# Performance work log

Hardware: AMD Instinct MI355X
Metric: run time of the kernel (lower is better)

Reference implementation:

```python
import jax, jax.numpy as jnp
import numpy as np
from jax.scipy.linalg import expm

LAMBDA_ORTHO = 1.0


def setup_inputs() -> dict:
    key = jax.random.key(0)
    so8_raw = jax.random.normal(key, (524288, 8, 8), dtype=jnp.float32)
    return {"so8_raw": so8_raw}


def reference(so8_raw):
    # A = 0.5 * (P - P^T): skew-symmetric part per 8x8 block
    A = 0.5 * (so8_raw - jnp.swapaxes(so8_raw, -1, -2))
    # R = expm(A), batched over leading dim via vmap
    R = jax.vmap(expm)(A)
    # ||R^T R - I||_F per block, then mean over blocks
    gram = jnp.einsum('nji,njk->nik', R, R)  # R^T R, [N,8,8]
    err = gram - jnp.eye(8, dtype=R.dtype)
    ortho_err = jnp.sqrt(jnp.sum(err * err, axis=(1, 2))).mean()
    return LAMBDA_ORTHO * ortho_err
```

## Files before the change

### kernel.cpp

```cpp
#include <hip/hip_runtime.h>
#include <math.h>

#pragma clang fp contract(off)

typedef float f2 __attribute__((ext_vector_type(2)));

static __device__ __forceinline__ f2 sp(float x) { f2 r; r.x = x; r.y = x; return r; }
#define FMA2(A, B, C) __builtin_elementwise_fma((A), (B), (C))

#define EL(m, i, j) (m[(i)*4 + ((j) >> 1)][(j) & 1])

__device__ __forceinline__ void mm8p(const f2* __restrict__ A,
                                     const f2* __restrict__ B,
                                     f2* __restrict__ C) {
  #pragma unroll
  for (int i = 0; i < 8; ++i) {
    #pragma unroll
    for (int c = 0; c < 4; ++c) {
      f2 s = sp(EL(A, i, 0)) * B[0*4 + c];
      #pragma unroll
      for (int k = 1; k < 8; ++k)
        s = FMA2(sp(EL(A, i, k)), B[k*4 + c], s);
      C[i*4 + c] = s;
    }
  }
}

__global__ __launch_bounds__(256, 1)
void triality_kernel(const float* __restrict__ in, double* __restrict__ acc)
{
  const int t = blockIdx.x * 256 + threadIdx.x;
  const float4* src = (const float4*)(in + (size_t)t * 64);

  float p[64];
  #pragma unroll
  for (int i = 0; i < 16; ++i) {
    float4 q4 = src[i];
    p[4*i+0] = q4.x; p[4*i+1] = q4.y; p[4*i+2] = q4.z; p[4*i+3] = q4.w;
  }

  f2 aa[32];
  #pragma unroll
  for (int i = 0; i < 8; ++i)
    #pragma unroll
    for (int j = 0; j < 8; ++j)
      EL(aa, i, j) = 0.5f * (p[i*8+j] - p[j*8+i]);

  float l1 = 0.0f;
  #pragma unroll
  for (int j = 0; j < 8; ++j) {
    float cs = 0.0f;
    #pragma unroll
    for (int i = 0; i < 8; ++i) cs = cs + fabsf(EL(aa, i, j));
    l1 = fmaxf(l1, cs);
  }

  float fl = floorf(log2f(l1 / 3.925724783138660f));
  int ns = (fl > 0.0f) ? (int)fl : 0;
  if (ns > 0) {
    f2 sc = sp(exp2f((float)(-ns)));
    #pragma unroll
    for (int e = 0; e < 32; ++e) aa[e] = aa[e] * sc;
  }

  f2 a2[32];
  #pragma unroll
  for (int i = 0; i < 8; ++i)
    #pragma unroll
    for (int c = 0; c < 4; ++c) {
      f2 s = sp(EL(aa, i, 0)) * aa[0*4 + c];
      #pragma unroll
      for (int k = 1; k < 8; ++k)
        s = FMA2(sp(EL(aa, i, k)), aa[k*4 + c], s);
      a2[i*4 + c] = s;
    }

  f2 a4[32];
  #pragma unroll
  for (int i = 0; i < 8; ++i)
    #pragma unroll
    for (int c = 0; c < 4; ++c) {
      f2 s = sp(EL(a2, i, 0)) * a2[0*4 + c];
      #pragma unroll
      for (int k = 1; k < 8; ++k)
        s = FMA2(sp(EL(a2, i, k)), a2[k*4 + c], s);
      a4[i*4 + c] = s;
    }

  f2 w6[32];
  #pragma unroll
  for (int i = 0; i < 8; ++i)
    #pragma unroll
    for (int c = 0; c < 4; ++c) {
      f2 s = sp(EL(a4, i, 0)) * a2[0*4 + c];
      #pragma unroll
      for (int k = 1; k < 8; ++k)
        s = FMA2(sp(EL(a4, i, k)), a2[k*4 + c], s);
      w6[i*4 + c] = s;
    }

  f2 vv[32];
  #pragma unroll
  for (int e = 0; e < 32; ++e) {
    f2 x6 = w6[e], x4 = a4[e], x2 = a2[e];
    f2 w = FMA2(sp(1512.0f), x4, x6);
    w = FMA2(sp(277200.0f), x2, w);
    f2 v = FMA2(sp(56.0f), x6, sp(25200.0f) * x4);
    v = FMA2(sp(1995840.0f), x2, v);
    w6[e] = w; vv[e] = v;
  }
  #pragma unroll
  for (int i = 0; i < 8; ++i) {
    EL(w6, i, i) = EL(w6, i, i) + 8648640.0f;
    EL(vv, i, i) = EL(vv, i, i) + 17297280.0f;
  }

  f2 uu[32];
  #pragma unroll
  for (int i = 0; i < 8; ++i)
    #pragma unroll
    for (int c = 0; c < 4; ++c) {
      f2 s = sp(EL(aa, i, 0)) * w6[0*4 + c];
      #pragma unroll
      for (int k = 1; k < 8; ++k)
        s = FMA2(sp(EL(aa, i, k)), w6[k*4 + c], s);
      uu[i*4 + c] = s;
    }

  #pragma unroll
  for (int e = 0; e < 32; ++e) {
    f2 U = uu[e], V = vv[e];
    uu[e] = U + V;
    vv[e] = V - U;
  }
  f2* P = uu;
  f2* Q = vv;

  #pragma unroll
  for (int k = 0; k < 8; ++k) {
    float amax = fabsf(EL(Q, k, k)); int jp = k;
    #pragma unroll
    for (int i = k+1; i < 8; ++i) {
      float av = fabsf(EL(Q, i, k));
      if (av > amax) { amax = av; jp = i; }
    }
    #pragma unroll
    for (int i = k+1; i < 8; ++i) {
      bool d = (jp == i);
      #pragma unroll
      for (int j = 0; j < 8; ++j) {
        float x = EL(Q, k, j), y = EL(Q, i, j);
        EL(Q, k, j) = d ? y : x;
        EL(Q, i, j) = d ? x : y;
        float px = EL(P, k, j), py = EL(P, i, j);
        EL(P, k, j) = d ? py : px;
        EL(P, i, j) = d ? px : py;
      }
    }
    float dk = EL(Q, k, k);
    #pragma unroll
    for (int i = k+1; i < 8; ++i) EL(Q, i, k) = EL(Q, i, k) / dk;
    #pragma unroll
    for (int i = k+1; i < 8; ++i) {
      float lik = EL(Q, i, k);
      #pragma unroll
      for (int j = k+1; j < 8; ++j)
        EL(Q, i, j) = __builtin_fmaf(-lik, EL(Q, k, j), EL(Q, i, j));
      f2 nl = sp(-lik);
      #pragma unroll
      for (int c = 0; c < 4; ++c)
        P[i*4 + c] = FMA2(nl, P[k*4 + c], P[i*4 + c]);
    }
  }

  #pragma unroll
  for (int k = 7; k >= 0; --k) {
    float dk = EL(Q, k, k);
    #pragma unroll
    for (int j = 0; j < 8; ++j) EL(P, k, j) = EL(P, k, j) / dk;
    #pragma unroll
    for (int i = 0; i < k; ++i) {
      f2 nu = sp(-EL(Q, i, k));
      #pragma unroll
      for (int c = 0; c < 4; ++c)
        P[i*4 + c] = FMA2(nu, P[k*4 + c], P[i*4 + c]);
    }
  }

  for (int sq = 0; sq < ns; ++sq) {
    f2 t2[32];
    mm8p(P, P, t2);
    #pragma unroll
    for (int e = 0; e < 32; ++e) P[e] = t2[e];
  }

  f2 s2p = sp(0.0f);
  #pragma unroll
  for (int i = 0; i < 8; ++i) {
    #pragma unroll
    for (int c = 0; c < 4; ++c) {
      f2 g = sp(EL(P, 0, i)) * P[0*4 + c];
      #pragma unroll
      for (int j = 1; j < 8; ++j)
        g = FMA2(sp(EL(P, j, i)), P[j*4 + c], g);
      f2 idv; idv.x = (2*c == i) ? 1.0f : 0.0f; idv.y = (2*c + 1 == i) ? 1.0f : 0.0f;
      f2 e = g - idv;
      s2p = FMA2(e, e, s2p);
    }
  }
  float frob = sqrtf(s2p.x + s2p.y);

  double dv = (double)frob;
  #pragma unroll
  for (int off = 32; off > 0; off >>= 1)
    dv += __shfl_down(dv, off);

  __shared__ double part[4];
  const int lane = threadIdx.x & 63;
  const int wid  = threadIdx.x >> 6;
  if (lane == 0) part[wid] = dv;
  __syncthreads();
  if (threadIdx.x == 0) {
    double s = (part[0] + part[1]) + (part[2] + part[3]);
    atomicAdd(acc, s);
  }
}

__global__ void finalize_kernel(const double* __restrict__ acc,
                                float* __restrict__ out, int nmat)
{
  out[0] = (float)(acc[0] / (double)nmat);
}

extern "C" void kernel_launch(void* const* d_in, const int* in_sizes, int n_in,
                              void* d_out, int out_size, void* d_ws, size_t ws_size,
                              hipStream_t stream) {
  const float* in = (const float*)d_in[0];
  float* out = (float*)d_out;
  double* acc = (double*)d_ws;
  int nmat = in_sizes[0] / 64;
  hipMemsetAsync(d_ws, 0, sizeof(double), stream);
  triality_kernel<<<nmat / 256, 256, 0, stream>>>(in, acc);
  finalize_kernel<<<1, 1, 0, stream>>>(acc, out, nmat);
}
```

Before: 219.0 us.

## Exploit skew/symmetric structure of A powers and spill A to LDS to cut registers

Stores the skew-symmetric A as 28 packed values, computes only the upper half of the symmetric A^2 and mirrors it, and keeps A^4 as a packed 36-element symmetric array. A is parked in shared memory during the polynomial evaluation and reloaded for the U product. The pivot swap becomes a row-select with temporaries, the Gram error sum uses symmetry to halve the work, and occupancy is raised via waves_per_eu(5). The aim is fewer FLOPs and lower register pressure so more waves can run, at the cost of extra LDS traffic and possible spills.

```diff
diff --git a/kernel.cpp b/kernel.cpp
--- a/kernel.cpp
+++ b/kernel.cpp
@@ -6,9 +6,17 @@
 typedef float f2 __attribute__((ext_vector_type(2)));
 
 static __device__ __forceinline__ f2 sp(float x) { f2 r; r.x = x; r.y = x; return r; }
+static __device__ __forceinline__ f2 sel2(bool d, f2 a, f2 b) {
+  f2 r; r.x = d ? a.x : b.x; r.y = d ? a.y : b.y; return r;
+}
 #define FMA2(A, B, C) __builtin_elementwise_fma((A), (B), (C))
 
 #define EL(m, i, j) (m[(i)*4 + ((j) >> 1)][(j) & 1])
+
+#define UA(i, j) ((((i) * (15 - (i))) / 2) + (j) - (i) - 1)
+#define U4(i, j) ((((i) * (17 - (i))) / 2) + (j) - (i))
+#define A4P(i, k) ((i) <= (k) ? a4p[U4(i, k)] : a4p[U4(k, i)])
+#define ELA(i, k) ((i) < (k) ? ar[UA(i, k)] : ((i) > (k) ? -ar[UA(k, i)] : 0.0f))
 
 __device__ __forceinline__ void mm8p(const f2* __restrict__ A,
                                      const f2* __restrict__ B,
@@ -26,9 +34,12 @@
   }
 }
 
-__global__ __launch_bounds__(256, 1)
+__global__ __launch_bounds__(256) __attribute__((amdgpu_waves_per_eu(5)))
 void triality_kernel(const float* __restrict__ in, double* __restrict__ acc)
 {
+  __shared__ float sap[256][29];
+  __shared__ double part[4];
+
   const int t = blockIdx.x * 256 + threadIdx.x;
   const float4* src = (const float4*)(in + (size_t)t * 64);
 
@@ -39,132 +50,174 @@
     p[4*i+0] = q4.x; p[4*i+1] = q4.y; p[4*i+2] = q4.z; p[4*i+3] = q4.w;
   }
 
-  f2 aa[32];
-  #pragma unroll
-  for (int i = 0; i < 8; ++i)
-    #pragma unroll
-    for (int j = 0; j < 8; ++j)
-      EL(aa, i, j) = 0.5f * (p[i*8+j] - p[j*8+i]);
+  float ap[28];
+  #pragma unroll
+  for (int i = 0; i < 8; ++i)
+    #pragma unroll
+    for (int j = i + 1; j < 8; ++j)
+      ap[UA(i, j)] = 0.5f * (p[i*8 + j] - p[j*8 + i]);
 
   float l1 = 0.0f;
   #pragma unroll
   for (int j = 0; j < 8; ++j) {
     float cs = 0.0f;
     #pragma unroll
-    for (int i = 0; i < 8; ++i) cs = cs + fabsf(EL(aa, i, j));
+    for (int i = 0; i < 8; ++i) {
+      if (i < j)      cs = cs + fabsf(ap[UA(i, j)]);
+      else if (i > j) cs = cs + fabsf(ap[UA(j, i)]);
+    }
     l1 = fmaxf(l1, cs);
   }
 
   float fl = floorf(log2f(l1 / 3.925724783138660f));
   int ns = (fl > 0.0f) ? (int)fl : 0;
   if (ns > 0) {
-    f2 sc = sp(exp2f((float)(-ns)));
-    #pragma unroll
-    for (int e = 0; e < 32; ++e) aa[e] = aa[e] * sc;
-  }
+    float sc = exp2f((float)(-ns));
+    #pragma unroll
+    for (int m = 0; m < 28; ++m) ap[m] = ap[m] * sc;
+  }
+
+  f2 af[32];
+  #pragma unroll
+  for (int i = 0; i < 8; ++i)
+    #pragma unroll
+    for (int j = 0; j < 8; ++j)
+      EL(af, i, j) = (i < j) ? ap[UA(i, j)]
+                   : ((i > j) ? -ap[UA(j, i)] : 0.0f);
+
+  #pragma unroll
+  for (int m = 0; m < 28; ++m) sap[threadIdx.x][m] = ap[m];
+  asm volatile("" ::: "memory");
 
   f2 a2[32];
   #pragma unroll
   for (int i = 0; i < 8; ++i)
     #pragma unroll
     for (int c = 0; c < 4; ++c) {
-      f2 s = sp(EL(aa, i, 0)) * aa[0*4 + c];
+      if (2*c + 1 >= i) {
+        f2 s = sp(EL(af, i, 0)) * af[0*4 + c];
+        #pragma unroll
+        for (int k = 1; k < 8; ++k)
+          s = FMA2(sp(EL(af, i, k)), af[k*4 + c], s);
+        a2[i*4 + c] = s;
+      }
+    }
+  #pragma unroll
+  for (int i = 0; i < 8; ++i)
+    #pragma unroll
+    for (int c = 0; c < 4; ++c)
+      if (2*c + 1 < i) {
+        EL(a2, i, 2*c)     = EL(a2, 2*c,     i);
+        EL(a2, i, 2*c + 1) = EL(a2, 2*c + 1, i);
+      }
+
+  float a4p[36];
+  #pragma unroll
+  for (int i = 0; i < 8; ++i)
+    #pragma unroll
+    for (int j = i; j < 8; ++j) {
+      float s = EL(a2, i, 0) * EL(a2, 0, j);
       #pragma unroll
       for (int k = 1; k < 8; ++k)
-        s = FMA2(sp(EL(aa, i, k)), aa[k*4 + c], s);
-      a2[i*4 + c] = s;
-    }
-
-  f2 a4[32];
-  #pragma unroll
-  for (int i = 0; i < 8; ++i)
-    #pragma unroll
-    for (int c = 0; c < 4; ++c) {
-      f2 s = sp(EL(a2, i, 0)) * a2[0*4 + c];
+        s = __builtin_fmaf(EL(a2, i, k), EL(a2, k, j), s);
+      a4p[U4(i, j)] = s;
+    }
+
+  f2 a6[32];
+  #pragma unroll
+  for (int i = 0; i < 8; ++i)
+    #pragma unroll
+    for (int c = 0; c < 4; ++c) {
+      f2 s = sp(A4P(i, 0)) * a2[0*4 + c];
       #pragma unroll
       for (int k = 1; k < 8; ++k)
-        s = FMA2(sp(EL(a2, i, k)), a2[k*4 + c], s);
-      a4[i*4 + c] = s;
-    }
-
-  f2 w6[32];
-  #pragma unroll
-  for (int i = 0; i < 8; ++i)
-    #pragma unroll
-    for (int c = 0; c < 4; ++c) {
-      f2 s = sp(EL(a4, i, 0)) * a2[0*4 + c];
+        s = FMA2(sp(A4P(i, k)), a2[k*4 + c], s);
+      a6[i*4 + c] = s;
+    }
+
+  #pragma unroll
+  for (int i = 0; i < 8; ++i)
+    #pragma unroll
+    for (int c = 0; c < 4; ++c) {
+      f2 x2 = a2[i*4 + c], x6 = a6[i*4 + c];
+      f2 x4; x4.x = A4P(i, 2*c); x4.y = A4P(i, 2*c + 1);
+      f2 w = FMA2(sp(1512.0f), x4, x6);
+      w = FMA2(sp(277200.0f), x2, w);
+      f2 v = FMA2(sp(56.0f), x6, sp(25200.0f) * x4);
+      v = FMA2(sp(1995840.0f), x2, v);
+      a6[i*4 + c] = w;
+      a2[i*4 + c] = v;
+    }
+  #pragma unroll
+  for (int i = 0; i < 8; ++i) {
+    EL(a6, i, i) = EL(a6, i, i) + 8648640.0f;
+    EL(a2, i, i) = EL(a2, i, i) + 17297280.0f;
+  }
+
+  asm volatile("" ::: "memory");
+  float ar[28];
+  #pragma unroll
+  for (int m = 0; m < 28; ++m) ar[m] = sap[threadIdx.x][m];
+
+  f2 pp[32];
+  #pragma unroll
+  for (int c = 0; c < 4; ++c)
+    #pragma unroll
+    for (int i = 0; i < 8; ++i) {
+      f2 s = sp(ELA(i, 0)) * a6[0*4 + c];
       #pragma unroll
       for (int k = 1; k < 8; ++k)
-        s = FMA2(sp(EL(a4, i, k)), a2[k*4 + c], s);
-      w6[i*4 + c] = s;
-    }
-
-  f2 vv[32];
-  #pragma unroll
-  for (int e = 0; e < 32; ++e) {
-    f2 x6 = w6[e], x4 = a4[e], x2 = a2[e];
-    f2 w = FMA2(sp(1512.0f), x4, x6);
-    w = FMA2(sp(277200.0f), x2, w);
-    f2 v = FMA2(sp(56.0f), x6, sp(25200.0f) * x4);
-    v = FMA2(sp(1995840.0f), x2, v);
-    w6[e] = w; vv[e] = v;
-  }
-  #pragma unroll
-  for (int i = 0; i < 8; ++i) {
-    EL(w6, i, i) = EL(w6, i, i) + 8648640.0f;
-    EL(vv, i, i) = EL(vv, i, i) + 17297280.0f;
-  }
-
-  f2 uu[32];
-  #pragma unroll
-  for (int i = 0; i < 8; ++i)
-    #pragma unroll
-    for (int c = 0; c < 4; ++c) {
-      f2 s = sp(EL(aa, i, 0)) * w6[0*4 + c];
-      #pragma unroll
-      for (int k = 1; k < 8; ++k)
-        s = FMA2(sp(EL(aa, i, k)), w6[k*4 + c], s);
-      uu[i*4 + c] = s;
-    }
-
-  #pragma unroll
-  for (int e = 0; e < 32; ++e) {
-    f2 U = uu[e], V = vv[e];
-    uu[e] = U + V;
-    vv[e] = V - U;
-  }
-  f2* P = uu;
-  f2* Q = vv;
+        s = FMA2(sp(ELA(i, k)), a6[k*4 + c], s);
+      f2 V = a2[i*4 + c];
+      pp[i*4 + c] = s + V;
+      a2[i*4 + c] = V - s;
+    }
+  f2* P = pp;
+  f2* Q = a2;
 
   #pragma unroll
   for (int k = 0; k < 8; ++k) {
     float amax = fabsf(EL(Q, k, k)); int jp = k;
     #pragma unroll
-    for (int i = k+1; i < 8; ++i) {
+    for (int i = k + 1; i < 8; ++i) {
       float av = fabsf(EL(Q, i, k));
       if (av > amax) { amax = av; jp = i; }
     }
-    #pragma unroll
-    for (int i = k+1; i < 8; ++i) {
+    const int c0 = k >> 1;
+    f2 rkq[4], rkp[4], tq[4], tp[4];
+    #pragma unroll
+    for (int c = c0; c < 4; ++c) { rkq[c] = Q[k*4 + c]; tq[c] = rkq[c]; }
+    #pragma unroll
+    for (int c = 0; c < 4; ++c)  { rkp[c] = P[k*4 + c]; tp[c] = rkp[c]; }
+    #pragma unroll
+    for (int i = k + 1; i < 8; ++i) {
       bool d = (jp == i);
       #pragma unroll
-      for (int j = 0; j < 8; ++j) {
-        float x = EL(Q, k, j), y = EL(Q, i, j);
-        EL(Q, k, j) = d ? y : x;
-        EL(Q, i, j) = d ? x : y;
-        float px = EL(P, k, j), py = EL(P, i, j);
-        EL(P, k, j) = d ? py : px;
-        EL(P, i, j) = d ? px : py;
-      }
-    }
+      for (int c = c0; c < 4; ++c) {
+        f2 qi = Q[i*4 + c];
+        tq[c] = sel2(d, qi, tq[c]);
+        Q[i*4 + c] = sel2(d, rkq[c], qi);
+      }
+      #pragma unroll
+      for (int c = 0; c < 4; ++c) {
+        f2 pi = P[i*4 + c];
+        tp[c] = sel2(d, pi, tp[c]);
+        P[i*4 + c] = sel2(d, rkp[c], pi);
+      }
+    }
+    #pragma unroll
+    for (int c = c0; c < 4; ++c) Q[k*4 + c] = tq[c];
+    #pragma unroll
+    for (int c = 0; c < 4; ++c)  P[k*4 + c] = tp[c];
+
     float dk = EL(Q, k, k);
     #pragma unroll
-    for (int i = k+1; i < 8; ++i) EL(Q, i, k) = EL(Q, i, k) / dk;
-    #pragma unroll
-    for (int i = k+1; i < 8; ++i) {
+    for (int i = k + 1; i < 8; ++i) EL(Q, i, k) = EL(Q, i, k) / dk;
+    #pragma unroll
+    for (int i = k + 1; i < 8; ++i) {
       float lik = EL(Q, i, k);
       #pragma unroll
-      for (int j = k+1; j < 8; ++j)
+      for (int j = k + 1; j < 8; ++j)
         EL(Q, i, j) = __builtin_fmaf(-lik, EL(Q, k, j), EL(Q, i, j));
       f2 nl = sp(-lik);
       #pragma unroll
@@ -199,13 +252,19 @@
   for (int i = 0; i < 8; ++i) {
     #pragma unroll
     for (int c = 0; c < 4; ++c) {
-      f2 g = sp(EL(P, 0, i)) * P[0*4 + c];
-      #pragma unroll
-      for (int j = 1; j < 8; ++j)
-        g = FMA2(sp(EL(P, j, i)), P[j*4 + c], g);
-      f2 idv; idv.x = (2*c == i) ? 1.0f : 0.0f; idv.y = (2*c + 1 == i) ? 1.0f : 0.0f;
-      f2 e = g - idv;
-      s2p = FMA2(e, e, s2p);
+      if (2*c + 1 >= i) {
+        f2 g = sp(EL(P, 0, i)) * P[0*4 + c];
+        #pragma unroll
+        for (int j = 1; j < 8; ++j)
+          g = FMA2(sp(EL(P, j, i)), P[j*4 + c], g);
+        f2 idv; idv.x = (2*c == i) ? 1.0f : 0.0f;
+        idv.y = (2*c + 1 == i) ? 1.0f : 0.0f;
+        f2 e = g - idv;
+        f2 we;
+        we.x = (2*c > i) ? (e.x + e.x) : ((2*c == i) ? e.x : 0.0f);
+        we.y = (2*c + 1 == i) ? e.y : (e.y + e.y);
+        s2p = FMA2(we, e, s2p);
+      }
     }
   }
   float frob = sqrtf(s2p.x + s2p.y);
@@ -215,7 +274,6 @@
   for (int off = 32; off > 0; off >>= 1)
     dv += __shfl_down(dv, off);
 
-  __shared__ double part[4];
   const int lane = threadIdx.x & 63;
   const int wid  = threadIdx.x >> 6;
   if (lane == 0) part[wid] = dv;
```

After: 605.6 us. 177% more time.
